# Optimization experiments

Hardware: AMD Instinct MI355X
Metric: run time of the kernel (lower is better)

## Reference

```python
import jax, jax.numpy as jnp
import numpy as np

N = 4096      # vertices (ring graph)
R = 3         # ring connectivity radius -> n = 2R+1 = 7 neighbors (incl. self)
C0, C1, C2 = 16, 32, 32


def _build_graph():
    v = np.arange(N)

    def rfield(l):
        off = np.arange(-l * R, l * R + 1)
        return np.sort((v[:, None] + off[None, :]) % N, axis=1)  # [N, 2lR+1]

    rf0, rf1, rf2 = rfield(0), rfield(1), rfield(2)
    nbrs = rf1  # neighborhood(v, 1), sorted, includes v

    def chi_idx(rf_v, rf_prev):
        # position of each element of v's rfield inside each neighbor's prev rfield
        rfp = rf_prev[nbrs]                                   # [N, n, Kp]
        eq = rf_v[:, None, :, None] == rfp[:, :, None, :]     # [N, n, K, Kp]
        mask = eq.any(-1).astype(np.float32)                  # element present?
        idx = eq.argmax(-1).astype(np.int32)                  # gather index (0 if absent)
        return idx, mask

    idx1, mask1 = chi_idx(rf1, rf0)
    idx2, mask2 = chi_idx(rf2, rf1)

    def sub_adj(rf):
        d = np.abs(rf[:, :, None] - rf[:, None, :])
        d = np.minimum(d, N - d)
        return ((d >= 1) & (d <= R)).astype(np.float32)       # [N, K, K]

    return nbrs.astype(np.int32), idx1, mask1, idx2, mask2, sub_adj(rf1), sub_adj(rf2)


def setup_inputs() -> dict:
    key = jax.random.key(0)
    ks = jax.random.split(key, 10)
    nbrs, idx1, mask1, idx2, mask2, adj1, adj2 = _build_graph()
    return {
        "labels": jax.random.normal(ks[0], (N, C0), jnp.float32),
        "nbrs": jnp.asarray(nbrs),
        "idx1": jnp.asarray(idx1), "mask1": jnp.asarray(mask1),
        "idx2": jnp.asarray(idx2), "mask2": jnp.asarray(mask2),
        "adj1": jnp.asarray(adj1), "adj2": jnp.asarray(adj2),
        "W1": jax.random.normal(ks[1], (C1, C0), jnp.float32) * 0.1,
        "b1": jax.random.normal(ks[2], (C1,), jnp.float32) * 0.1,
        "W2": jax.random.normal(ks[3], (C2, C1), jnp.float32) * 0.1,
        "b2": jax.random.normal(ks[4], (C2,), jnp.float32) * 0.1,
        "al1": jax.random.normal(ks[5], (1,), jnp.float32),
        "al2": jax.random.normal(ks[6], (1,), jnp.float32),
        "Wfc": jax.random.normal(ks[7], (1, C2), jnp.float32) * 0.1,
        "bfc": jax.random.normal(ks[8], (1,), jnp.float32) * 0.1,
    }


def _level(feat_prev, nbrs, idx, mask, adj, al, W, b):
    # feat_prev: [N, C, Kp, Kp]; idx/mask: [N, n, K]; adj: [N, K, K]
    g = feat_prev[nbrs]                                          # [N, n, C, Kp, Kp]
    g = jnp.take_along_axis(g, idx[:, :, None, :, None], axis=3)  # [N, n, C, K, Kp]
    g = jnp.take_along_axis(g, idx[:, :, None, None, :], axis=4)  # [N, n, C, K, K]
    g = g * mask[:, :, None, :, None] * mask[:, :, None, None, :]  # chi F chi^T
    agg = g.sum(axis=1) + al * adj[:, None, :, :]                # [N, C, K, K]
    n_, C, K, _ = agg.shape
    x = agg.reshape(n_, K * K, C)            # faithful to torch .view(k*k, -1)
    y = jax.nn.relu(x @ W.T + b)             # [N, K*K, Cout]
    return y.reshape(n_, W.shape[0], K, K)   # faithful to torch .view(out, k, k)


def reference(labels, nbrs, idx1, mask1, idx2, mask2, adj1, adj2,
              W1, b1, W2, b2, al1, al2, Wfc, bfc):
    feat0 = labels.reshape(N, C0, 1, 1)
    f1 = _level(feat0, nbrs, idx1, mask1, adj1, al1, W1, b1)
    f2 = _level(f1, nbrs, idx2, mask2, adj2, al2, W2, b2)
    g_repr = f2.sum(axis=(2, 3)).sum(axis=0, keepdims=True)      # [1, C2]
    output = g_repr @ Wfc.T + bfc                                # [1, 1]
    return output, g_repr
```

## Files before the change

### kernel.cpp

```cpp
#include <hip/hip_runtime.h>

#define NV 4096
#define NMASK 4095
#define NN 7
#define KK1 49
#define KK2 169
#define C0 16
#define C1 32
#define C2 32
#define F1LEN 1568
#define RSTR 882
#define QSTR 18
#define VB 4
#define NB (NV / VB)
#define NT 704
#define WROWS 10
#define LROWS 16
#define TIL 31

typedef unsigned int uint;
typedef unsigned short ushort;
typedef unsigned char uchar;
typedef __attribute__((ext_vector_type(8))) short short8v;
typedef __attribute__((ext_vector_type(4))) float float4v;

static __device__ __forceinline__ ushort f2bf(float f) {
    __bf16 h = (__bf16)f;
    union { __bf16 h; ushort u; } v; v.h = h;
    return v.u;
}
static __device__ __forceinline__ float bflo(uint w) { return __uint_as_float(w << 16); }
static __device__ __forceinline__ float bfhi(uint w) { return __uint_as_float(w & 0xffff0000u); }

struct PermT { ushort v[176]; };
static constexpr PermT make_perm() {
    PermT p{};
    int idx = 0;
    for (int c = 7; c >= 0; --c)
        for (int i = 0; i < 13; ++i)
            for (int j = 0; j < 13; ++j) {
                int mn = i < j ? i : j, mx = i < j ? j : i;
                int lo = (mx - 9 < -3) ? -3 : mx - 9;
                int hi = (mn - 3 > 3) ? 3 : mn - 3;
                int cnt = hi - lo + 1; if (cnt < 0) cnt = 0;
                if (cnt == c) { p.v[idx] = (ushort)((c << 8) | (i << 4) | j); ++idx; }
            }
    return p;
}
__device__ constexpr PermT PERM = make_perm();

__global__ __launch_bounds__(704) void fused_kernel(
    const float* __restrict__ labels, const int* __restrict__ nbrs,
    const float* __restrict__ mask1, const int* __restrict__ idx2,
    const float* __restrict__ mask2, const float* __restrict__ adj1,
    const float* __restrict__ adj2, const float* __restrict__ W1,
    const float* __restrict__ b1, const float* __restrict__ W2,
    const float* __restrict__ b2, const float* __restrict__ al1,
    const float* __restrict__ al2, float* __restrict__ gpart)
{
    __shared__ __align__(16) uint   fs[WROWS * RSTR];
    __shared__ __align__(16) ushort aggT[VB * 5408];
    __shared__ float m2s[VB][91];
    __shared__ uchar i2q[VB][96];
    __shared__ int   rowOf2[VB][NN];
    __shared__ float grs[32];
    __shared__ float al1s, al2s;

    ushort* aggf16 = aggT;
    float* Lw   = (float*)((char*)aggT + 15680);
    float* m1w  = (float*)((char*)aggT + 16704);
    int*   nbrW = (int*)  ((char*)aggT + 18664);
    ushort* lutB = (ushort*)((char*)aggT + 20480);

    int t = threadIdx.x;
    int v0 = blockIdx.x * VB;
    int lane = t & 63, wvid = t >> 6;
    int r16 = lane & 15, kg = lane >> 4;
    bool interior = (v0 >= 6) && (v0 + 9 <= NMASK);

    if (t < 32) grs[t] = 0.f;
    if (t == 0) { al1s = al1[0]; al2s = al2[0]; }
    for (int e = t; e < LROWS * 16; e += NT)
        Lw[e] = labels[(size_t)(((v0 - 6 + (e >> 4)) + NV) & NMASK) * 16 + (e & 15)];
    for (int e = t; e < F1LEN; e += NT) {
        int c = e / 49, q = e - c * 49;
        int w = (c >> 1) ^ ((q >> 4) << 1);
        lutB[e] = (ushort)((q * QSTR + w) * 2 + (c & 1));
    }
    if (!interior) {
        for (int e = t; e < WROWS * 49; e += NT)
            m1w[e] = mask1[(size_t)(((v0 - 3 + e / 49) + NV) & NMASK) * 49 + (e % 49)];
        for (int e = t; e < WROWS * NN; e += NT) {
            int r = e / NN, u = e % NN;
            nbrW[e] = (nbrs[(size_t)(((v0 - 3 + r) + NV) & NMASK) * NN + u] - v0 + 6 + NV) & NMASK;
        }
        for (int e = t; e < VB * 91; e += NT) {
            int vl = e / 91, x = e % 91;
            m2s[vl][x] = mask2[(size_t)v0 * 91 + e];
            i2q[vl][x] = (uchar)idx2[(size_t)v0 * 91 + e];
        }
        for (int e = t; e < VB * NN; e += NT)
            rowOf2[e / NN][e % NN] = (nbrs[v0 * NN + e] - v0 + 3 + NV) & NMASK;
    }
    __syncthreads();

    if (interior) {
        if (t < WROWS * 49) {
            int r = t / 49, ij = t % 49, i = ij / 7, j = ij % 7;
            int ad = i - j; ad = ad < 0 ? -ad : ad;
            ushort* dst = aggf16 + r * 784 + ij;
            if (ad == 0) {
                const float* lr = &Lw[(r + i) * 16];
                #pragma unroll
                for (int c = 0; c < 16; ++c) dst[c * 49] = f2bf(lr[c]);
            } else {
                ushort v = (ad <= 3) ? f2bf(al1s) : (ushort)0;
                #pragma unroll
                for (int c = 0; c < 16; ++c) dst[c * 49] = v;
            }
        }
    } else if (t < WROWS * 49) {
        int r = t / 49, ij = t % 49, i = ij / 7, j = ij % 7;
        float a[16];
        #pragma unroll
        for (int c = 0; c < 16; ++c) a[c] = 0.f;
        #pragma unroll
        for (int u = 0; u < NN; ++u) {
            float mm = m1w[r * 49 + u * 7 + i] * m1w[r * 49 + u * 7 + j];
            const float4* lr = (const float4*)&Lw[nbrW[r * 7 + u] * 16];
            float4 l0 = lr[0], l1 = lr[1], l2 = lr[2], l3 = lr[3];
            a[0]+=mm*l0.x; a[1]+=mm*l0.y; a[2]+=mm*l0.z; a[3]+=mm*l0.w;
            a[4]+=mm*l1.x; a[5]+=mm*l1.y; a[6]+=mm*l1.z; a[7]+=mm*l1.w;
            a[8]+=mm*l2.x; a[9]+=mm*l2.y; a[10]+=mm*l2.z; a[11]+=mm*l2.w;
            a[12]+=mm*l3.x; a[13]+=mm*l3.y; a[14]+=mm*l3.z; a[15]+=mm*l3.w;
        }
        float av = al1s * adj1[(size_t)(((v0 - 3 + r) + NV) & NMASK) * 49 + ij];
        #pragma unroll
        for (int c = 0; c < 16; ++c)
            aggf16[r * 784 + c * 49 + ij] = f2bf(a[c] + av);
    }
    __syncthreads();

    {
        short8v wb0, wb1;
        #pragma unroll
        for (int e = 0; e < 8; ++e) {
            int k = kg * 8 + e;
            wb0[e] = (k < 16) ? (short)f2bf(W1[r16 * 16 + k]) : (short)0;
            wb1[e] = (k < 16) ? (short)f2bf(W1[(r16 + 16) * 16 + k]) : (short)0;
        }
        float bb0 = b1[r16], bb1 = b1[r16 + 16];
        ushort* fsh = (ushort*)fs;
        for (int tile = wvid; tile < TIL; tile += 11) {
            int m = tile * 16 + r16;
            short8v a;
            #pragma unroll
            for (int e = 0; e < 8; ++e) a[e] = 0;
            if (kg < 2 && m < WROWS * 49) {
                int r = m / 49, p = m - r * 49;
                uint4 araw = *(const uint4*)((const uint*)aggf16 + r * 392 + p * 8 + kg * 4);
                a = *reinterpret_cast<short8v*>(&araw);
            }
            float4v z = {0.f, 0.f, 0.f, 0.f};
            float4v d0 = __builtin_amdgcn_mfma_f32_16x16x32_bf16(a, wb0, z, 0, 0, 0);
            float4v d1 = __builtin_amdgcn_mfma_f32_16x16x32_bf16(a, wb1, z, 0, 0, 0);
            #pragma unroll
            for (int rr = 0; rr < 4; ++rr) {
                int m2v = tile * 16 + kg * 4 + rr;
                if (m2v < WROWS * 49) {
                    int r = m2v / 49, p = m2v - r * 49;
                    int f2a = p * 32 + r16;
                    int rb = r * (RSTR * 2);
                    fsh[rb + lutB[f2a]]      = f2bf(fmaxf(d0[rr] + bb0, 0.f));
                    fsh[rb + lutB[f2a + 16]] = f2bf(fmaxf(d1[rr] + bb1, 0.f));
                }
            }
        }
    }
    __syncthreads();

    if (t < VB * KK2) {
        int vl = t & 3, s = t >> 2;
        uint cell = PERM.v[s];
        int i = (cell >> 4) & 15, j = cell & 15;
        int ij = i * 13 + j;
        int cnt, dlo;
        if (interior) {
            cnt = cell >> 8;
            int mn = i < j ? i : j, mx = i < j ? j : i;
            dlo = (mx - 9 < -3) ? -3 : mx - 9;
        } else { cnt = 7; dlo = 0; }
        float acc[32];
        #pragma unroll
        for (int c = 0; c < 32; ++c) acc[c] = 0.f;
        #pragma unroll
        for (int n = 0; n < 7; ++n) {
            if (n < cnt) {
                float mm; int q, row;
                if (interior) {
                    int d = dlo + n;
                    q = (i - 3 - d) * 7 + (j - 3 - d);
                    row = vl + 3 + d;
                    mm = 1.f;
                } else {
                    mm = m2s[vl][n * 13 + i] * m2s[vl][n * 13 + j];
                    q = (int)i2q[vl][n * 13 + i] * 7 + (int)i2q[vl][n * 13 + j];
                    row = rowOf2[vl][n];
                }
                const uint* base = fs + row * RSTR + q * QSTR;
                int sw = (q >> 4) << 1;
                #pragma unroll
                for (int e = 0; e < 8; ++e) {
                    uint2 dd = *(const uint2*)(base + ((2 * e) ^ sw));
                    acc[4*e+0] += mm * bflo(dd.x);
                    acc[4*e+1] += mm * bfhi(dd.x);
                    acc[4*e+2] += mm * bflo(dd.y);
                    acc[4*e+3] += mm * bfhi(dd.y);
                }
            }
        }
        float av;
        if (interior) {
            int adiff = i > j ? i - j : j - i;
            av = (adiff >= 1 && adiff <= 3) ? al2s : 0.f;
        } else {
            av = al2s * adj2[(size_t)(v0 + vl) * KK2 + ij];
        }
        #pragma unroll
        for (int c = 0; c < 32; ++c)
            aggT[vl * 5408 + c * KK2 + ij] = f2bf(acc[c] + av);
    }
    __syncthreads();

    {
        short8v cb0, cb1;
        #pragma unroll
        for (int e = 0; e < 8; ++e) {
            cb0[e] = (short)f2bf(W2[r16 * 32 + kg * 8 + e]);
            cb1[e] = (short)f2bf(W2[(r16 + 16) * 32 + kg * 8 + e]);
        }
        float bias0 = b2[r16], bias1 = b2[r16 + 16];
        int p0 = wvid * 16;
        int prow = p0 + r16; if (prow > 168) prow = 168;
        float s0[4] = {0.f,0.f,0.f,0.f}, s1[4] = {0.f,0.f,0.f,0.f};
        #pragma unroll
        for (int vl = 0; vl < VB; ++vl) {
            uint4 araw = *(const uint4*)((const char*)aggT + vl * 10816 + prow * 64 + kg * 16);
            short8v a = *reinterpret_cast<short8v*>(&araw);
            float4v z = {0.f, 0.f, 0.f, 0.f};
            float4v d0 = __builtin_amdgcn_mfma_f32_16x16x32_bf16(a, cb0, z, 0, 0, 0);
            float4v d1 = __builtin_amdgcn_mfma_f32_16x16x32_bf16(a, cb1, z, 0, 0, 0);
            #pragma unroll
            for (int r = 0; r < 4; ++r) {
                s0[r] += fmaxf(d0[r] + bias0, 0.f);
                s1[r] += fmaxf(d1[r] + bias1, 0.f);
            }
        }
        int chA = (p0 * 32) / KK2;
        float part0 = 0.f, part1 = 0.f, part2 = 0.f, part3 = 0.f;
        #pragma unroll
        for (int r = 0; r < 4; ++r) {
            int p = p0 + kg * 4 + r;
            if (p < KK2) {
                int c0 = (p * 32 + r16) / KK2 - chA;
                part0 += (c0 == 0) ? s0[r] : 0.f;
                part1 += (c0 == 1) ? s0[r] : 0.f;
                part2 += (c0 == 2) ? s0[r] : 0.f;
                part3 += (c0 == 3) ? s0[r] : 0.f;
                int c1 = (p * 32 + r16 + 16) / KK2 - chA;
                part0 += (c1 == 0) ? s1[r] : 0.f;
                part1 += (c1 == 1) ? s1[r] : 0.f;
                part2 += (c1 == 2) ? s1[r] : 0.f;
                part3 += (c1 == 3) ? s1[r] : 0.f;
            }
        }
        #pragma unroll
        for (int off = 32; off > 0; off >>= 1) {
            part0 += __shfl_xor(part0, off);
            part1 += __shfl_xor(part1, off);
            part2 += __shfl_xor(part2, off);
            part3 += __shfl_xor(part3, off);
        }
        if (lane == 0) {
            atomicAdd(&grs[chA], part0);
            if (chA + 1 < 32) atomicAdd(&grs[chA + 1], part1);
            if (chA + 2 < 32) atomicAdd(&grs[chA + 2], part2);
            if (chA + 3 < 32) atomicAdd(&grs[chA + 3], part3);
        }
    }
    __syncthreads();
    if (t < 32) gpart[blockIdx.x * 32 + t] = grs[t];
}

__global__ __launch_bounds__(1024) void fc_kernel(
    const float* __restrict__ gpart, const float* __restrict__ Wfc,
    const float* __restrict__ bfc, float* __restrict__ out)
{
    __shared__ float red[32][33];
    int t = threadIdx.x;
    int ch = t & 31, seg = t >> 5;
    float s = 0.f;
    for (int b = seg; b < NB; b += 32) s += gpart[b * 32 + ch];
    red[seg][ch] = s;
    __syncthreads();
    if (t < 32) {
        float g = 0.f;
        #pragma unroll
        for (int k = 0; k < 32; ++k) g += red[k][t];
        out[1 + t] = g;
        red[0][t] = g * Wfc[t];
    }
    __syncthreads();
    if (t == 0) {
        float p = bfc[0];
        #pragma unroll
        for (int k = 0; k < 32; ++k) p += red[0][k];
        out[0] = p;
    }
}

__global__ __launch_bounds__(64) void lvl1_kernel(
    const float* __restrict__ labels, const int* __restrict__ nbrs,
    const float* __restrict__ mask1, const float* __restrict__ adj1,
    const float* __restrict__ W1, const float* __restrict__ b1,
    const float* __restrict__ al1, float* __restrict__ f1out)
{
    __shared__ float Ls[NN][C0];
    __shared__ float m1s[NN][7];
    __shared__ float a1s[KK1];
    __shared__ float aggsh[C0 * KK1];
    __shared__ float W1s[C1 * 17];
    __shared__ float b1s[C1];
    int v = blockIdx.x, t = threadIdx.x;
    for (int e = t; e < NN * C0; e += 64) {
        int u = e >> 4, c = e & 15;
        Ls[u][c] = labels[(size_t)nbrs[v * NN + u] * C0 + c];
    }
    for (int e = t; e < KK1; e += 64) {
        m1s[e / 7][e % 7] = mask1[(size_t)v * KK1 + e];
        a1s[e] = adj1[(size_t)v * KK1 + e];
    }
    for (int e = t; e < C1 * C0; e += 64) W1s[(e >> 4) * 17 + (e & 15)] = W1[e];
    if (t < C1) b1s[t] = b1[t];
    float alpha = al1[0];
    __syncthreads();
    for (int e = t; e < C0 * KK1; e += 64) {
        int c = e / KK1, ij = e % KK1, i = ij / 7, j = ij % 7;
        float s = 0.f;
        #pragma unroll
        for (int u = 0; u < NN; ++u) s += Ls[u][c] * (m1s[u][i] * m1s[u][j]);
        aggsh[e] = s + alpha * a1s[ij];
    }
    __syncthreads();
    int co = t & 31;
    for (int e = t; e < F1LEN; e += 64) {
        int p = e >> 5;
        float s = b1s[co];
        #pragma unroll
        for (int c = 0; c < C0; ++c) s += aggsh[p * C0 + c] * W1s[co * 17 + c];
        f1out[(size_t)v * F1LEN + e] = fmaxf(s, 0.f);
    }
}

#define F1PAD 56
#define AGPAD 177
__global__ __launch_bounds__(192) void lvl2_kernel(
    const float* __restrict__ f1, const int* __restrict__ nbrs,
    const int* __restrict__ idx2, const float* __restrict__ mask2,
    const float* __restrict__ adj2, const float* __restrict__ W2,
    const float* __restrict__ b2, const float* __restrict__ al2,
    float* __restrict__ gr)
{
    __shared__ float f1s[C1 * F1PAD];
    __shared__ float aggT2[C1 * AGPAD];
    __shared__ float W2s[C2 * C1];
    __shared__ float b2s[C2];
    __shared__ float grs[C2];
    __shared__ int nbs[NN];
    int v = blockIdx.x, t = threadIdx.x;
    if (t < NN) nbs[t] = nbrs[v * NN + t];
    if (t < C2) { b2s[t] = b2[t]; grs[t] = 0.f; }
    for (int e = t; e < C2 * C1; e += 192) W2s[e] = W2[e];
    float alpha = al2[0];
    bool act = (t < KK2);
    float mmr[NN]; int qr[NN];
    float acc[C1];
    if (act) {
        int i = t / 13, j = t % 13;
        const float* mbase = mask2 + (size_t)v * NN * 13;
        const int* ibase = idx2 + (size_t)v * NN * 13;
        #pragma unroll
        for (int u = 0; u < NN; ++u) {
            mmr[u] = mbase[u * 13 + i] * mbase[u * 13 + j];
            qr[u] = ibase[u * 13 + i] * 7 + ibase[u * 13 + j];
        }
    }
    #pragma unroll
    for (int c = 0; c < C1; ++c) acc[c] = 0.f;
    int dst[9]; int nd = 0;
    for (int e = t; e < F1LEN; e += 192) dst[nd++] = (e / 49) * F1PAD + (e % 49);
    for (int u = 0; u < NN; ++u) {
        __syncthreads();
        const float* src = f1 + (size_t)nbs[u] * F1LEN;
        { int k = 0; for (int e = t; e < F1LEN; e += 192) f1s[dst[k++]] = src[e]; }
        __syncthreads();
        if (act) {
            float mv = mmr[u]; int q = qr[u];
            #pragma unroll
            for (int c = 0; c < C1; ++c) acc[c] += mv * f1s[c * F1PAD + q];
        }
    }
    if (act) {
        float a2v = alpha * adj2[(size_t)v * KK2 + t];
        #pragma unroll
        for (int c = 0; c < C1; ++c) {
            int f = c * KK2 + t;
            aggT2[(f & 31) * AGPAD + (f >> 5)] = acc[c] + a2v;
        }
    }
    __syncthreads();
    if (act) {
        int p = t;
        float ar[C1];
        #pragma unroll
        for (int c2 = 0; c2 < C1; ++c2) ar[c2] = aggT2[c2 * AGPAD + p];
        int chA = (p * 32) / KK2;
        int csplit = KK2 - (p * 32 - chA * KK2);
        float sA = 0.f, sB = 0.f;
        #pragma unroll
        for (int co = 0; co < C2; ++co) {
            float s = b2s[co];
            #pragma unroll
            for (int k = 0; k < 8; ++k) {
                float4 wv = *(const float4*)(&W2s[co * C1 + 4 * k]);
                s += ar[4*k+0]*wv.x + ar[4*k+1]*wv.y + ar[4*k+2]*wv.z + ar[4*k+3]*wv.w;
            }
            s = fmaxf(s, 0.f);
            if (co < csplit) sA += s; else sB += s;
        }
        atomicAdd(&grs[chA], sA);
        if (csplit < 32) atomicAdd(&grs[chA + 1], sB);
    }
    __syncthreads();
    if (t < C2) atomicAdd(&gr[t], grs[t]);
}

__global__ __launch_bounds__(64) void fc_small_kernel(
    const float* __restrict__ gr, const float* __restrict__ Wfc,
    const float* __restrict__ bfc, float* __restrict__ out)
{
    int t = threadIdx.x;
    float g = (t < C2) ? gr[t] : 0.f;
    if (t < C2) out[1 + t] = g;
    float p = (t < C2) ? g * Wfc[t] : 0.f;
    #pragma unroll
    for (int off = 32; off > 0; off >>= 1) p += __shfl_down(p, off);
    if (t == 0) out[0] = p + bfc[0];
}

extern "C" void kernel_launch(void* const* d_in, const int* in_sizes, int n_in,
                              void* d_out, int out_size, void* d_ws, size_t ws_size,
                              hipStream_t stream)
{
    const float* labels = (const float*)d_in[0];
    const int*   nbrs   = (const int*)d_in[1];
    const float* mask1  = (const float*)d_in[3];
    const int*   idx2   = (const int*)d_in[4];
    const float* mask2  = (const float*)d_in[5];
    const float* adj1   = (const float*)d_in[6];
    const float* adj2   = (const float*)d_in[7];
    const float* W1     = (const float*)d_in[8];
    const float* b1     = (const float*)d_in[9];
    const float* W2     = (const float*)d_in[10];
    const float* b2     = (const float*)d_in[11];
    const float* al1    = (const float*)d_in[12];
    const float* al2    = (const float*)d_in[13];
    const float* Wfc    = (const float*)d_in[14];
    const float* bfc    = (const float*)d_in[15];

    if (ws_size >= (size_t)NB * 32 * sizeof(float)) {
        float* gpart = (float*)d_ws;
        fused_kernel<<<NB, NT, 0, stream>>>(labels, nbrs, mask1, idx2, mask2,
                                            adj1, adj2, W1, b1, W2, b2, al1, al2, gpart);
        fc_kernel<<<1, 1024, 0, stream>>>(gpart, Wfc, bfc, (float*)d_out);
    } else {
        float* f1 = (float*)d_ws;
        float* gr = (float*)((char*)d_ws + (size_t)NV * F1LEN * sizeof(float));
        hipMemsetAsync(gr, 0, C2 * sizeof(float), stream);
        lvl1_kernel<<<NV, 64, 0, stream>>>(labels, nbrs, mask1, adj1, W1, b1, al1, f1);
        lvl2_kernel<<<NV, 192, 0, stream>>>(f1, nbrs, idx2, mask2, adj2, W2, b2, al2, gr);
        fc_small_kernel<<<1, 64, 0, stream>>>(gr, Wfc, bfc, (float*)d_out);
    }
}
```

Measured before the change: 50.20 us.

## Fuse final FC reduction into main kernel via atomic last-block pattern

Replaces the separate fc_kernel launch with global atomics: each block adds its per-channel partial sums into a padded workspace, and the last block to bump a counter computes the final outputs. A memset clears the accumulators before launch. The level-2 aggregation accumulators are also rewritten as float2 vectors so the compiler can emit packed FMA instructions. The goal is to remove a kernel launch and the partial-buffer round trip, at the cost of atomic contention, a memset, and possible memory-ordering risk because there is no explicit fence before the counter increment.

```diff
diff --git a/kernel.cpp b/kernel.cpp
--- a/kernel.cpp
+++ b/kernel.cpp
@@ -23,6 +23,7 @@
 typedef unsigned char uchar;
 typedef __attribute__((ext_vector_type(8))) short short8v;
 typedef __attribute__((ext_vector_type(4))) float float4v;
+typedef __attribute__((ext_vector_type(2))) float f32x2;
 
 static __device__ __forceinline__ ushort f2bf(float f) {
     __bf16 h = (__bf16)f;
@@ -56,7 +57,9 @@
     const float* __restrict__ adj2, const float* __restrict__ W1,
     const float* __restrict__ b1, const float* __restrict__ W2,
     const float* __restrict__ b2, const float* __restrict__ al1,
-    const float* __restrict__ al2, float* __restrict__ gpart)
+    const float* __restrict__ al2, const float* __restrict__ Wfc,
+    const float* __restrict__ bfc, float* __restrict__ grws,
+    uint* __restrict__ cnt, float* __restrict__ out)
 {
     __shared__ __align__(16) uint   fs[WROWS * RSTR];
     __shared__ __align__(16) ushort aggT[VB * 5408];
@@ -184,18 +187,18 @@
         uint cell = PERM.v[s];
         int i = (cell >> 4) & 15, j = cell & 15;
         int ij = i * 13 + j;
-        int cnt, dlo;
+        int cnt_, dlo;
         if (interior) {
-            cnt = cell >> 8;
+            cnt_ = cell >> 8;
             int mn = i < j ? i : j, mx = i < j ? j : i;
             dlo = (mx - 9 < -3) ? -3 : mx - 9;
-        } else { cnt = 7; dlo = 0; }
-        float acc[32];
-        #pragma unroll
-        for (int c = 0; c < 32; ++c) acc[c] = 0.f;
+        } else { cnt_ = 7; dlo = 0; }
+        f32x2 acc2[16];
+        #pragma unroll
+        for (int c = 0; c < 16; ++c) acc2[c] = (f32x2){0.f, 0.f};
         #pragma unroll
         for (int n = 0; n < 7; ++n) {
-            if (n < cnt) {
+            if (n < cnt_) {
                 float mm; int q, row;
                 if (interior) {
                     int d = dlo + n;
@@ -207,15 +210,16 @@
                     q = (int)i2q[vl][n * 13 + i] * 7 + (int)i2q[vl][n * 13 + j];
                     row = rowOf2[vl][n];
                 }
+                f32x2 mm2 = {mm, mm};
                 const uint* base = fs + row * RSTR + q * QSTR;
                 int sw = (q >> 4) << 1;
                 #pragma unroll
                 for (int e = 0; e < 8; ++e) {
                     uint2 dd = *(const uint2*)(base + ((2 * e) ^ sw));
-                    acc[4*e+0] += mm * bflo(dd.x);
-                    acc[4*e+1] += mm * bfhi(dd.x);
-                    acc[4*e+2] += mm * bflo(dd.y);
-                    acc[4*e+3] += mm * bfhi(dd.y);
+                    f32x2 x0 = {bflo(dd.x), bfhi(dd.x)};
+                    f32x2 x1 = {bflo(dd.y), bfhi(dd.y)};
+                    acc2[2 * e]     += mm2 * x0;
+                    acc2[2 * e + 1] += mm2 * x1;
                 }
             }
         }
@@ -227,8 +231,10 @@
             av = al2s * adj2[(size_t)(v0 + vl) * KK2 + ij];
         }
         #pragma unroll
-        for (int c = 0; c < 32; ++c)
-            aggT[vl * 5408 + c * KK2 + ij] = f2bf(acc[c] + av);
+        for (int c = 0; c < 16; ++c) {
+            aggT[vl * 5408 + (2 * c) * KK2 + ij]     = f2bf(acc2[c][0] + av);
+            aggT[vl * 5408 + (2 * c + 1) * KK2 + ij] = f2bf(acc2[c][1] + av);
+        }
     }
     __syncthreads();
 
@@ -289,33 +295,22 @@
         }
     }
     __syncthreads();
-    if (t < 32) gpart[blockIdx.x * 32 + t] = grs[t];
-}
-
-__global__ __launch_bounds__(1024) void fc_kernel(
-    const float* __restrict__ gpart, const float* __restrict__ Wfc,
-    const float* __restrict__ bfc, float* __restrict__ out)
-{
-    __shared__ float red[32][33];
-    int t = threadIdx.x;
-    int ch = t & 31, seg = t >> 5;
-    float s = 0.f;
-    for (int b = seg; b < NB; b += 32) s += gpart[b * 32 + ch];
-    red[seg][ch] = s;
-    __syncthreads();
-    if (t < 32) {
-        float g = 0.f;
-        #pragma unroll
-        for (int k = 0; k < 32; ++k) g += red[k][t];
-        out[1 + t] = g;
-        red[0][t] = g * Wfc[t];
-    }
-    __syncthreads();
-    if (t == 0) {
-        float p = bfc[0];
-        #pragma unroll
-        for (int k = 0; k < 32; ++k) p += red[0][k];
-        out[0] = p;
+
+    if (t < 32) atomicAdd(&grws[t * 32], grs[t]);
+    __syncthreads();
+
+    if (t < 64) {
+        uint tick = 0;
+        if (t == 0) tick = atomicAdd(cnt, 1u);
+        tick = (uint)__shfl((int)tick, 0);
+        if (tick == NB - 1) {
+            float g = (t < 32) ? atomicAdd(&grws[t * 32], 0.0f) : 0.f;
+            if (t < 32) out[1 + t] = g;
+            float pd = (t < 32) ? g * Wfc[t] : 0.f;
+            #pragma unroll
+            for (int off = 32; off > 0; off >>= 1) pd += __shfl_down(pd, off);
+            if (t == 0) out[0] = pd + bfc[0];
+        }
     }
 }
 
@@ -478,11 +473,15 @@
     const float* Wfc    = (const float*)d_in[14];
     const float* bfc    = (const float*)d_in[15];
 
-    if (ws_size >= (size_t)NB * 32 * sizeof(float)) {
-        float* gpart = (float*)d_ws;
+    const size_t comm_bytes = 32 * 32 * sizeof(float) + 64;
+
+    if (ws_size >= comm_bytes) {
+        float* grws = (float*)d_ws;
+        uint*  cnt  = (uint*)((char*)d_ws + 32 * 32 * sizeof(float));
+        hipMemsetAsync(d_ws, 0, comm_bytes, stream);
         fused_kernel<<<NB, NT, 0, stream>>>(labels, nbrs, mask1, idx2, mask2,
-                                            adj1, adj2, W1, b1, W2, b2, al1, al2, gpart);
-        fc_kernel<<<1, 1024, 0, stream>>>(gpart, Wfc, bfc, (float*)d_out);
+                                            adj1, adj2, W1, b1, W2, b2, al1, al2,
+                                            Wfc, bfc, grws, cnt, (float*)d_out);
     } else {
         float* f1 = (float*)d_ws;
         float* gr = (float*)((char*)d_ws + (size_t)NV * F1LEN * sizeof(float));
```

Measured after the change: 49.07 us. 1.02x faster.
